# Kernel tuning notes

Hardware: AMD Instinct MI355X
Metric: run time of the kernel (lower is better)

## Reference

```python
import jax, jax.numpy as jnp
import numpy as np
import math

HEAD = 8
D_MODEL = 512
D_K = D_MODEL // HEAD
BS = 1024
HIST = 199


def setup_inputs() -> dict:
    key = jax.random.key(0)
    ks = jax.random.split(key, 9)
    s = 1.0 / math.sqrt(D_MODEL)
    return {
        "current_embed": jax.random.normal(ks[0], (BS, D_MODEL), dtype=jnp.float32),
        "previous_embed": jax.random.normal(ks[1], (BS, HIST, D_MODEL), dtype=jnp.float32),
        "local_attn_mask": jax.random.normal(ks[2], (BS, HIST + 1), dtype=jnp.float32),
        "Wq": jax.random.normal(ks[3], (D_MODEL, D_MODEL), dtype=jnp.float32) * s,
        "bq": jax.random.normal(ks[4], (D_MODEL,), dtype=jnp.float32) * s,
        "Wk": jax.random.normal(ks[5], (D_MODEL, D_MODEL), dtype=jnp.float32) * s,
        "bk": jax.random.normal(ks[6], (D_MODEL,), dtype=jnp.float32) * s,
        "Wv": jax.random.normal(ks[7], (D_MODEL, D_MODEL), dtype=jnp.float32) * s,
        "bv": jax.random.normal(ks[8], (D_MODEL,), dtype=jnp.float32) * s,
    }


def reference(current_embed, previous_embed, local_attn_mask, Wq, bq, Wk, bk, Wv, bv):
    bs = current_embed.shape[0]
    # all_time_embed: [bs, T, d] where T = hist + 1
    all_time = jnp.concatenate([previous_embed, current_embed[:, None, :]], axis=1)
    T = all_time.shape[1]
    # Q: single query per batch -> [bs, head, d_k]
    q = (current_embed @ Wq.T + bq).reshape(bs, HEAD, D_K)
    # K, V over full history -> [bs, T, head, d_k]
    k = (all_time @ Wk.T + bk).reshape(bs, T, HEAD, D_K)
    v = (all_time @ Wv.T + bv).reshape(bs, T, HEAD, D_K)
    # scores: [bs, head, T], scaled; additive mask broadcast over heads
    scores = jnp.einsum("bhd,bthd->bht", q, k) / math.sqrt(D_K)
    norm = jax.nn.softmax(scores + local_attn_mask[:, None, :], axis=-1)
    # weighted sum over time -> [bs, head, d_k] -> [bs, d_model]
    out = jnp.einsum("bht,bthd->bhd", norm, v)
    return out.reshape(bs, D_MODEL)
```

## Files before the change

kernel.cpp:

```cpp
#include <hip/hip_runtime.h>
#include <math.h>

#define DM 512
#define NH 8
#define BS 1024
#define HIST 199
#define TT 200

__device__ __forceinline__ float dot8(const float4& a0, const float4& a1,
                                      const float4& b0, const float4& b1) {
  float p = a0.x * b0.x;
  p = fmaf(a0.y, b0.y, p);
  p = fmaf(a0.z, b0.z, p);
  p = fmaf(a0.w, b0.w, p);
  p = fmaf(a1.x, b1.x, p);
  p = fmaf(a1.y, b1.y, p);
  p = fmaf(a1.z, b1.z, p);
  p = fmaf(a1.w, b1.w, p);
  return p;
}

__device__ __forceinline__ float wred64(float p) {
  p += __shfl_xor(p, 1);
  p += __shfl_xor(p, 2);
  p += __shfl_xor(p, 4);
  p += __shfl_xor(p, 8);
  p += __shfl_xor(p, 16);
  p += __shfl_xor(p, 32);
  return p;
}

__global__ __launch_bounds__(256, 4) void qproj_kernel(
    const float* __restrict__ cur, const float* __restrict__ Wq,
    const float* __restrict__ bq, float* __restrict__ q) {
  const int lane = threadIdx.x & 63;
  const int wave = threadIdx.x >> 6;
  const int bg = blockIdx.x >> 2;
  const int jq = blockIdx.x & 3;
  const int j0 = jq * 128 + wave * 32;
  float4 ca[4], cb[4];
#pragma unroll
  for (int bb = 0; bb < 4; ++bb) {
    const float* cp = cur + (size_t)(bg * 4 + bb) * DM;
    ca[bb] = *(const float4*)(cp + 4 * lane);
    cb[bb] = *(const float4*)(cp + 256 + 4 * lane);
  }
  float keep[2] = {0.f, 0.f};
  for (int r = 0; r < 32; ++r) {
    const float* wp = Wq + (size_t)(j0 + r) * DM;
    const float4 wa = *(const float4*)(wp + 4 * lane);
    const float4 wb = *(const float4*)(wp + 256 + 4 * lane);
    float pp[4];
#pragma unroll
    for (int bb = 0; bb < 4; ++bb)
      pp[bb] = wred64(dot8(ca[bb], cb[bb], wa, wb));
#pragma unroll
    for (int bb = 0; bb < 4; ++bb)
      if (lane == ((bb & 1) * 32 + r)) keep[bb >> 1] = pp[bb];
  }
  const int r = lane & 31, bh = lane >> 5;
  const int j = j0 + r;
#pragma unroll
  for (int s = 0; s < 2; ++s) {
    const int b = bg * 4 + 2 * s + bh;
    q[(size_t)b * DM + j] = keep[s] + bq[j];
  }
}

__global__ __launch_bounds__(256, 4) void qk_kernel(
    const float* __restrict__ q, const float* __restrict__ Wk,
    const float* __restrict__ bk, float* __restrict__ qk1,
    float* __restrict__ qc1) {
  __shared__ float q8[8][64];
  const int tid = threadIdx.x;
  const int bg = blockIdx.x >> 3;
  const int h = blockIdx.x & 7;
  for (int i = tid; i < 512; i += 256) {
    const int bl = i >> 6, d = i & 63;
    q8[bl][d] = q[(size_t)(bg * 8 + bl) * DM + h * 64 + d];
  }
  __syncthreads();
  float acc0[8], acc1[8];
#pragma unroll
  for (int bl = 0; bl < 8; ++bl) {
    acc0[bl] = 0.f;
    acc1[bl] = 0.f;
  }
  const int e = tid;
  const float* wkb = Wk + (size_t)h * 64 * DM;
  for (int d4 = 0; d4 < 64; d4 += 4) {
    float w0[4], w1[4];
#pragma unroll
    for (int dd = 0; dd < 4; ++dd) {
      w0[dd] = wkb[(size_t)(d4 + dd) * DM + e];
      w1[dd] = wkb[(size_t)(d4 + dd) * DM + e + 256];
    }
#pragma unroll
    for (int bl = 0; bl < 8; ++bl) {
      const float4 qq = *(const float4*)&q8[bl][d4];
      acc0[bl] = fmaf(qq.x, w0[0], acc0[bl]);
      acc0[bl] = fmaf(qq.y, w0[1], acc0[bl]);
      acc0[bl] = fmaf(qq.z, w0[2], acc0[bl]);
      acc0[bl] = fmaf(qq.w, w0[3], acc0[bl]);
      acc1[bl] = fmaf(qq.x, w1[0], acc1[bl]);
      acc1[bl] = fmaf(qq.y, w1[1], acc1[bl]);
      acc1[bl] = fmaf(qq.z, w1[2], acc1[bl]);
      acc1[bl] = fmaf(qq.w, w1[3], acc1[bl]);
    }
  }
#pragma unroll
  for (int bl = 0; bl < 8; ++bl) {
    const size_t base = ((size_t)(bg * 8 + bl) * NH + h) * DM;
    qk1[base + e] = acc0[bl] * 0.125f;
    qk1[base + e + 256] = acc1[bl] * 0.125f;
  }
  if (tid < 8) {
    float s = 0.f;
    for (int d = 0; d < 64; ++d) s += q8[tid][d] * bk[h * 64 + d];
    qc1[(size_t)(bg * 8 + tid) * NH + h] = s * 0.125f;
  }
}

__global__ __launch_bounds__(512, 4) void attn_kernel(
    const float* __restrict__ cur, const float* __restrict__ prev,
    const float* __restrict__ mask, const float* __restrict__ qk1,
    const float* __restrict__ qc1, const float* __restrict__ Wv,
    const float* __restrict__ bv, float* __restrict__ out) {
  __shared__ float red[2][4][DM];
  __shared__ float lred[2][4][4];
  const int tid = threadIdx.x;
  const int lane = tid & 63;
  const int wave = tid >> 6;
  const int g = wave & 1;
  const int c = wave >> 1;
  const int b = blockIdx.x;

  float4 ka[4], kb[4];
  float qc[4];
#pragma unroll
  for (int hl = 0; hl < 4; ++hl) {
    const float* kp = qk1 + ((size_t)b * NH + (g * 4 + hl)) * DM;
    ka[hl] = *(const float4*)(kp + 4 * lane);
    kb[hl] = *(const float4*)(kp + 256 + 4 * lane);
    qc[hl] = qc1[(size_t)b * NH + (g * 4 + hl)];
  }
  float4 cA[4], cB[4];
#pragma unroll
  for (int hl = 0; hl < 4; ++hl) {
    cA[hl] = make_float4(0.f, 0.f, 0.f, 0.f);
    cB[hl] = make_float4(0.f, 0.f, 0.f, 0.f);
  }
  float ls0 = 0.f, ls1 = 0.f, ls2 = 0.f, ls3 = 0.f;
  const int t0 = c * 50;
  const int nrows = (c == 3) ? 49 : 50;
  const int ml = (lane < 49) ? lane : 49;
  const float mreg = mask[(size_t)b * TT + t0 + ml];

#define ATTN_ROW(RA, RB, MIDX)                                         \
  {                                                                    \
    float pp[4];                                                       \
    _Pragma("unroll") for (int hl = 0; hl < 4; ++hl) pp[hl] =          \
        dot8(RA, RB, ka[hl], kb[hl]);                                  \
    _Pragma("unroll") for (int hl = 0; hl < 4; ++hl) pp[hl] =          \
        wred64(pp[hl]);                                                \
    const float mval = __shfl(mreg, (MIDX));                           \
    _Pragma("unroll") for (int hl = 0; hl < 4; ++hl) {                 \
      const float w = __expf(pp[hl] + qc[hl] + mval);                  \
      if (hl == 0) ls0 += w;                                           \
      if (hl == 1) ls1 += w;                                           \
      if (hl == 2) ls2 += w;                                           \
      if (hl == 3) ls3 += w;                                           \
      cA[hl].x = fmaf(w, RA.x, cA[hl].x);                              \
      cA[hl].y = fmaf(w, RA.y, cA[hl].y);                              \
      cA[hl].z = fmaf(w, RA.z, cA[hl].z);                              \
      cA[hl].w = fmaf(w, RA.w, cA[hl].w);                              \
      cB[hl].x = fmaf(w, RB.x, cB[hl].x);                              \
      cB[hl].y = fmaf(w, RB.y, cB[hl].y);                              \
      cB[hl].z = fmaf(w, RB.z, cB[hl].z);                              \
      cB[hl].w = fmaf(w, RB.w, cB[hl].w);                              \
    }                                                                  \
  }

  const float* pa = prev + ((size_t)b * HIST + t0) * DM + 4 * lane;
  float4 r0a = *(const float4*)(pa);
  float4 r0b = *(const float4*)(pa + 256);
  float4 r1a = *(const float4*)(pa + DM);
  float4 r1b = *(const float4*)(pa + DM + 256);
  for (int i = 0; i < nrows; ++i) {
    int ip = i + 2;
    if (ip >= nrows) ip = nrows - 1;
    const float* np = pa + (size_t)ip * DM;
    const float4 q0a = *(const float4*)(np);
    const float4 q0b = *(const float4*)(np + 256);
    ATTN_ROW(r0a, r0b, i)
    r0a = r1a;
    r0b = r1b;
    r1a = q0a;
    r1b = q0b;
  }
  if (c == 3) {
    const float* cp = cur + (size_t)b * DM + 4 * lane;
    const float4 xa = *(const float4*)(cp);
    const float4 xb = *(const float4*)(cp + 256);
    ATTN_ROW(xa, xb, 49)
  }
#undef ATTN_ROW

  if (lane == 0) {
    lred[g][c][0] = ls0;
    lred[g][c][1] = ls1;
    lred[g][c][2] = ls2;
    lred[g][c][3] = ls3;
  }
  for (int cc = 0; cc < 4; ++cc) {
    if (c == cc) {
#pragma unroll
      for (int hl = 0; hl < 4; ++hl) {
        float* dst = &red[g][hl][0];
        if (cc == 0) {
          *(float4*)(dst + 4 * lane) = cA[hl];
          *(float4*)(dst + 256 + 4 * lane) = cB[hl];
        } else {
          float4 o0 = *(const float4*)(dst + 4 * lane);
          float4 o1 = *(const float4*)(dst + 256 + 4 * lane);
          o0.x += cA[hl].x;
          o0.y += cA[hl].y;
          o0.z += cA[hl].z;
          o0.w += cA[hl].w;
          o1.x += cB[hl].x;
          o1.y += cB[hl].y;
          o1.z += cB[hl].z;
          o1.w += cB[hl].w;
          *(float4*)(dst + 4 * lane) = o0;
          *(float4*)(dst + 256 + 4 * lane) = o1;
        }
      }
    }
    __syncthreads();
  }
  const int hh = wave;
  const int g2 = hh >> 2, h2 = hh & 3;
  const float linv = 1.0f / (lred[g2][0][h2] + lred[g2][1][h2] +
                             lred[g2][2][h2] + lred[g2][3][h2]);
  const float4 na = *(const float4*)(&red[g2][h2][0] + 4 * lane);
  const float4 nb = *(const float4*)(&red[g2][h2][0] + 256 + 4 * lane);
  float keep = 0.f;
  for (int r = 0; r < 64; ++r) {
    const float* wvp = Wv + (size_t)(hh * 64 + r) * DM;
    const float4 wa = *(const float4*)(wvp + 4 * lane);
    const float4 wb = *(const float4*)(wvp + 256 + 4 * lane);
    float p = wred64(dot8(na, nb, wa, wb));
    if (lane == r) keep = p;
  }
  out[(size_t)b * DM + hh * 64 + lane] = keep * linv + bv[hh * 64 + lane];
}

extern "C" void kernel_launch(void* const* d_in, const int* in_sizes, int n_in,
                              void* d_out, int out_size, void* d_ws,
                              size_t ws_size, hipStream_t stream) {
  const float* cur = (const float*)d_in[0];
  const float* prev = (const float*)d_in[1];
  const float* mask = (const float*)d_in[2];
  const float* Wq = (const float*)d_in[3];
  const float* bq = (const float*)d_in[4];
  const float* Wk = (const float*)d_in[5];
  const float* bk = (const float*)d_in[6];
  const float* Wv = (const float*)d_in[7];
  const float* bv = (const float*)d_in[8];
  float* out = (float*)d_out;

  float* q = (float*)d_ws;
  float* qk1 = q + (size_t)BS * DM;
  float* qc1 = qk1 + (size_t)BS * NH * DM;

  qproj_kernel<<<1024, 256, 0, stream>>>(cur, Wq, bq, q);
  qk_kernel<<<1024, 256, 0, stream>>>(q, Wk, bk, qk1, qc1);
  attn_kernel<<<1024, 512, 0, stream>>>(cur, prev, mask, qk1, qc1, Wv, bv, out);
}
```

Baseline: 681.8 us.

## Batch eight rows per step with transposed butterfly reduction of 32 partial dots

Processes history rows in blocks of 8. The 32 per-(head,row) partial dot products go through a transpose-style butterfly shuffle, so each lane ends up owning one reduced score and computes a single exp. Weights are then broadcast back by shuffle for the V accumulation. This replaces the per-row 4 full 6-step reductions and 4 exps with far fewer shuffles and one exp per lane per block. The cost is reloading each row from global/L2 twice, dropping the software prefetch, and higher register pressure from the 32-element arrays.

```diff
diff --git a/kernel.cpp b/kernel.cpp
--- a/kernel.cpp
+++ b/kernel.cpp
@@ -150,11 +150,78 @@
     cA[hl] = make_float4(0.f, 0.f, 0.f, 0.f);
     cB[hl] = make_float4(0.f, 0.f, 0.f, 0.f);
   }
-  float ls0 = 0.f, ls1 = 0.f, ls2 = 0.f, ls3 = 0.f;
+  float ls[4] = {0.f, 0.f, 0.f, 0.f};
   const int t0 = c * 50;
   const int nrows = (c == 3) ? 49 : 50;
   const int ml = (lane < 49) ? lane : 49;
   const float mreg = mask[(size_t)b * TT + t0 + ml];
+  const float* pa = prev + ((size_t)b * HIST + t0) * DM + 4 * lane;
+
+  const int h_l = (lane >> 3) & 3;
+  const int r_l = lane & 7;
+  const float qc_mine = qc1[(size_t)b * NH + g * 4 + h_l];
+
+  for (int ib = 0; ib < 6; ++ib) {
+    const int i0 = ib * 8;
+    float p[32];
+#pragma unroll
+    for (int rr = 0; rr < 8; ++rr) {
+      const float* rp = pa + (size_t)(i0 + rr) * DM;
+      const float4 ra = *(const float4*)rp;
+      const float4 rb = *(const float4*)(rp + 256);
+#pragma unroll
+      for (int hl = 0; hl < 4; ++hl)
+        p[hl * 8 + rr] = dot8(ra, rb, ka[hl], kb[hl]);
+    }
+    const int s1 = lane & 1, s2 = lane & 2, s4 = lane & 4;
+    const int s8 = lane & 8, s16 = lane & 16;
+    float t16[16];
+#pragma unroll
+    for (int k = 0; k < 16; ++k) {
+      const float a = p[2 * k], bb = p[2 * k + 1];
+      t16[k] = (s1 ? bb : a) + __shfl_xor(s1 ? a : bb, 1);
+    }
+    float t8[8];
+#pragma unroll
+    for (int k = 0; k < 8; ++k) {
+      const float a = t16[2 * k], bb = t16[2 * k + 1];
+      t8[k] = (s2 ? bb : a) + __shfl_xor(s2 ? a : bb, 2);
+    }
+    float t4[4];
+#pragma unroll
+    for (int k = 0; k < 4; ++k) {
+      const float a = t8[2 * k], bb = t8[2 * k + 1];
+      t4[k] = (s4 ? bb : a) + __shfl_xor(s4 ? a : bb, 4);
+    }
+    float t2[2];
+#pragma unroll
+    for (int k = 0; k < 2; ++k) {
+      const float a = t4[2 * k], bb = t4[2 * k + 1];
+      t2[k] = (s8 ? bb : a) + __shfl_xor(s8 ? a : bb, 8);
+    }
+    float sred = (s16 ? t2[1] : t2[0]) + __shfl_xor(s16 ? t2[0] : t2[1], 16);
+    sred += __shfl_xor(sred, 32);
+    const float w_mine = __expf(sred + qc_mine + __shfl(mreg, i0 + r_l));
+#pragma unroll
+    for (int rr = 0; rr < 8; ++rr) {
+      const float* rp = pa + (size_t)(i0 + rr) * DM;
+      const float4 ra = *(const float4*)rp;
+      const float4 rb = *(const float4*)(rp + 256);
+#pragma unroll
+      for (int hl = 0; hl < 4; ++hl) {
+        const float w = __shfl(w_mine, hl * 8 + rr);
+        ls[hl] += w;
+        cA[hl].x = fmaf(w, ra.x, cA[hl].x);
+        cA[hl].y = fmaf(w, ra.y, cA[hl].y);
+        cA[hl].z = fmaf(w, ra.z, cA[hl].z);
+        cA[hl].w = fmaf(w, ra.w, cA[hl].w);
+        cB[hl].x = fmaf(w, rb.x, cB[hl].x);
+        cB[hl].y = fmaf(w, rb.y, cB[hl].y);
+        cB[hl].z = fmaf(w, rb.z, cB[hl].z);
+        cB[hl].w = fmaf(w, rb.w, cB[hl].w);
+      }
+    }
+  }
 
 #define ATTN_ROW(RA, RB, MIDX)                                         \
   {                                                                    \
@@ -166,10 +233,7 @@
     const float mval = __shfl(mreg, (MIDX));                           \
     _Pragma("unroll") for (int hl = 0; hl < 4; ++hl) {                 \
       const float w = __expf(pp[hl] + qc[hl] + mval);                  \
-      if (hl == 0) ls0 += w;                                           \
-      if (hl == 1) ls1 += w;                                           \
-      if (hl == 2) ls2 += w;                                           \
-      if (hl == 3) ls3 += w;                                           \
+      ls[hl] += w;                                                     \
       cA[hl].x = fmaf(w, RA.x, cA[hl].x);                              \
       cA[hl].y = fmaf(w, RA.y, cA[hl].y);                              \
       cA[hl].z = fmaf(w, RA.z, cA[hl].z);                              \
@@ -181,22 +245,11 @@
     }                                                                  \
   }
 
-  const float* pa = prev + ((size_t)b * HIST + t0) * DM + 4 * lane;
-  float4 r0a = *(const float4*)(pa);
-  float4 r0b = *(const float4*)(pa + 256);
-  float4 r1a = *(const float4*)(pa + DM);
-  float4 r1b = *(const float4*)(pa + DM + 256);
-  for (int i = 0; i < nrows; ++i) {
-    int ip = i + 2;
-    if (ip >= nrows) ip = nrows - 1;
-    const float* np = pa + (size_t)ip * DM;
-    const float4 q0a = *(const float4*)(np);
-    const float4 q0b = *(const float4*)(np + 256);
-    ATTN_ROW(r0a, r0b, i)
-    r0a = r1a;
-    r0b = r1b;
-    r1a = q0a;
-    r1b = q0b;
+  for (int i = 48; i < nrows; ++i) {
+    const float* rp = pa + (size_t)i * DM;
+    const float4 ra = *(const float4*)rp;
+    const float4 rb = *(const float4*)(rp + 256);
+    ATTN_ROW(ra, rb, i)
   }
   if (c == 3) {
     const float* cp = cur + (size_t)b * DM + 4 * lane;
@@ -207,10 +260,10 @@
 #undef ATTN_ROW
 
   if (lane == 0) {
-    lred[g][c][0] = ls0;
-    lred[g][c][1] = ls1;
-    lred[g][c][2] = ls2;
-    lred[g][c][3] = ls3;
+    lred[g][c][0] = ls[0];
+    lred[g][c][1] = ls[1];
+    lred[g][c][2] = ls[2];
+    lred[g][c][3] = ls[3];
   }
   for (int cc = 0; cc < 4; ++cc) {
     if (c == cc) {
```

New measurement: 1.069 ms. +56.7%, slower.

## Assign one wave per head over all time steps, dropping cross-wave LDS reduction

Applied to the files above, without the earlier changes.

The attention kernel now gives each of the 8 waves one head and has it walk all 200 time rows, instead of splitting heads into two groups and time into four chunks per wave. This removes the serialized shared-memory reduction of partial context vectors and softmax sums, and the __syncthreads chain that went with it. In exchange, each block now reads every row of previous_embed eight times (once per wave), relying on L1/L2 reuse. The time loop is unrolled by two, the mask is staged in LDS, and launch bounds are raised to 8 blocks per CU for occupancy.

```diff
diff --git a/kernel.cpp b/kernel.cpp
--- a/kernel.cpp
+++ b/kernel.cpp
@@ -121,138 +121,84 @@
   }
 }
 
-__global__ __launch_bounds__(512, 4) void attn_kernel(
+__global__ __launch_bounds__(512, 8) void attn_kernel(
     const float* __restrict__ cur, const float* __restrict__ prev,
     const float* __restrict__ mask, const float* __restrict__ qk1,
     const float* __restrict__ qc1, const float* __restrict__ Wv,
     const float* __restrict__ bv, float* __restrict__ out) {
-  __shared__ float red[2][4][DM];
-  __shared__ float lred[2][4][4];
+  __shared__ float msk[TT];
   const int tid = threadIdx.x;
   const int lane = tid & 63;
-  const int wave = tid >> 6;
-  const int g = wave & 1;
-  const int c = wave >> 1;
+  const int h = tid >> 6;
   const int b = blockIdx.x;
 
-  float4 ka[4], kb[4];
-  float qc[4];
-#pragma unroll
-  for (int hl = 0; hl < 4; ++hl) {
-    const float* kp = qk1 + ((size_t)b * NH + (g * 4 + hl)) * DM;
-    ka[hl] = *(const float4*)(kp + 4 * lane);
-    kb[hl] = *(const float4*)(kp + 256 + 4 * lane);
-    qc[hl] = qc1[(size_t)b * NH + (g * 4 + hl)];
-  }
-  float4 cA[4], cB[4];
-#pragma unroll
-  for (int hl = 0; hl < 4; ++hl) {
-    cA[hl] = make_float4(0.f, 0.f, 0.f, 0.f);
-    cB[hl] = make_float4(0.f, 0.f, 0.f, 0.f);
-  }
-  float ls0 = 0.f, ls1 = 0.f, ls2 = 0.f, ls3 = 0.f;
-  const int t0 = c * 50;
-  const int nrows = (c == 3) ? 49 : 50;
-  const int ml = (lane < 49) ? lane : 49;
-  const float mreg = mask[(size_t)b * TT + t0 + ml];
-
-#define ATTN_ROW(RA, RB, MIDX)                                         \
-  {                                                                    \
-    float pp[4];                                                       \
-    _Pragma("unroll") for (int hl = 0; hl < 4; ++hl) pp[hl] =          \
-        dot8(RA, RB, ka[hl], kb[hl]);                                  \
-    _Pragma("unroll") for (int hl = 0; hl < 4; ++hl) pp[hl] =          \
-        wred64(pp[hl]);                                                \
-    const float mval = __shfl(mreg, (MIDX));                           \
-    _Pragma("unroll") for (int hl = 0; hl < 4; ++hl) {                 \
-      const float w = __expf(pp[hl] + qc[hl] + mval);                  \
-      if (hl == 0) ls0 += w;                                           \
-      if (hl == 1) ls1 += w;                                           \
-      if (hl == 2) ls2 += w;                                           \
-      if (hl == 3) ls3 += w;                                           \
-      cA[hl].x = fmaf(w, RA.x, cA[hl].x);                              \
-      cA[hl].y = fmaf(w, RA.y, cA[hl].y);                              \
-      cA[hl].z = fmaf(w, RA.z, cA[hl].z);                              \
-      cA[hl].w = fmaf(w, RA.w, cA[hl].w);                              \
-      cB[hl].x = fmaf(w, RB.x, cB[hl].x);                              \
-      cB[hl].y = fmaf(w, RB.y, cB[hl].y);                              \
-      cB[hl].z = fmaf(w, RB.z, cB[hl].z);                              \
-      cB[hl].w = fmaf(w, RB.w, cB[hl].w);                              \
-    }                                                                  \
-  }
-
-  const float* pa = prev + ((size_t)b * HIST + t0) * DM + 4 * lane;
+  for (int i = tid; i < TT; i += 512) msk[i] = mask[(size_t)b * TT + i];
+
+  const float* kp = qk1 + ((size_t)b * NH + h) * DM;
+  const float4 ka = *(const float4*)(kp + 4 * lane);
+  const float4 kb = *(const float4*)(kp + 256 + 4 * lane);
+  const float qc = qc1[(size_t)b * NH + h];
+  __syncthreads();
+
+  float4 cA = make_float4(0.f, 0.f, 0.f, 0.f);
+  float4 cB = make_float4(0.f, 0.f, 0.f, 0.f);
+  float ls = 0.f;
+
+#define ATTN_ROW(RA, RB, MV)                        \
+  {                                                 \
+    const float v = wred64(dot8(RA, RB, ka, kb));   \
+    const float w = __expf(v + qc + (MV));          \
+    ls += w;                                        \
+    cA.x = fmaf(w, RA.x, cA.x);                     \
+    cA.y = fmaf(w, RA.y, cA.y);                     \
+    cA.z = fmaf(w, RA.z, cA.z);                     \
+    cA.w = fmaf(w, RA.w, cA.w);                     \
+    cB.x = fmaf(w, RB.x, cB.x);                     \
+    cB.y = fmaf(w, RB.y, cB.y);                     \
+    cB.z = fmaf(w, RB.z, cB.z);                     \
+    cB.w = fmaf(w, RB.w, cB.w);                     \
+  }
+
+  const float* pa = prev + (size_t)b * HIST * DM + 4 * lane;
   float4 r0a = *(const float4*)(pa);
   float4 r0b = *(const float4*)(pa + 256);
   float4 r1a = *(const float4*)(pa + DM);
   float4 r1b = *(const float4*)(pa + DM + 256);
-  for (int i = 0; i < nrows; ++i) {
-    int ip = i + 2;
-    if (ip >= nrows) ip = nrows - 1;
-    const float* np = pa + (size_t)ip * DM;
-    const float4 q0a = *(const float4*)(np);
-    const float4 q0b = *(const float4*)(np + 256);
-    ATTN_ROW(r0a, r0b, i)
-    r0a = r1a;
-    r0b = r1b;
-    r1a = q0a;
-    r1b = q0b;
-  }
-  if (c == 3) {
+  for (int i = 0; i < 198; i += 2) {
+    const float* np0 = pa + (size_t)(i + 2) * DM;
+    int i3 = i + 3;
+    if (i3 > 198) i3 = 198;
+    const float* np1 = pa + (size_t)i3 * DM;
+    const float4 q0a = *(const float4*)(np0);
+    const float4 q0b = *(const float4*)(np0 + 256);
+    const float4 q1a = *(const float4*)(np1);
+    const float4 q1b = *(const float4*)(np1 + 256);
+    ATTN_ROW(r0a, r0b, msk[i])
+    ATTN_ROW(r1a, r1b, msk[i + 1])
+    r0a = q0a;
+    r0b = q0b;
+    r1a = q1a;
+    r1b = q1b;
+  }
+  ATTN_ROW(r0a, r0b, msk[198])
+  {
     const float* cp = cur + (size_t)b * DM + 4 * lane;
     const float4 xa = *(const float4*)(cp);
     const float4 xb = *(const float4*)(cp + 256);
-    ATTN_ROW(xa, xb, 49)
+    ATTN_ROW(xa, xb, msk[199])
   }
 #undef ATTN_ROW
 
-  if (lane == 0) {
-    lred[g][c][0] = ls0;
-    lred[g][c][1] = ls1;
-    lred[g][c][2] = ls2;
-    lred[g][c][3] = ls3;
-  }
-  for (int cc = 0; cc < 4; ++cc) {
-    if (c == cc) {
-#pragma unroll
-      for (int hl = 0; hl < 4; ++hl) {
-        float* dst = &red[g][hl][0];
-        if (cc == 0) {
-          *(float4*)(dst + 4 * lane) = cA[hl];
-          *(float4*)(dst + 256 + 4 * lane) = cB[hl];
-        } else {
-          float4 o0 = *(const float4*)(dst + 4 * lane);
-          float4 o1 = *(const float4*)(dst + 256 + 4 * lane);
-          o0.x += cA[hl].x;
-          o0.y += cA[hl].y;
-          o0.z += cA[hl].z;
-          o0.w += cA[hl].w;
-          o1.x += cB[hl].x;
-          o1.y += cB[hl].y;
-          o1.z += cB[hl].z;
-          o1.w += cB[hl].w;
-          *(float4*)(dst + 4 * lane) = o0;
-          *(float4*)(dst + 256 + 4 * lane) = o1;
-        }
-      }
-    }
-    __syncthreads();
-  }
-  const int hh = wave;
-  const int g2 = hh >> 2, h2 = hh & 3;
-  const float linv = 1.0f / (lred[g2][0][h2] + lred[g2][1][h2] +
-                             lred[g2][2][h2] + lred[g2][3][h2]);
-  const float4 na = *(const float4*)(&red[g2][h2][0] + 4 * lane);
-  const float4 nb = *(const float4*)(&red[g2][h2][0] + 256 + 4 * lane);
+  const float linv = 1.0f / ls;
   float keep = 0.f;
   for (int r = 0; r < 64; ++r) {
-    const float* wvp = Wv + (size_t)(hh * 64 + r) * DM;
+    const float* wvp = Wv + (size_t)(h * 64 + r) * DM;
     const float4 wa = *(const float4*)(wvp + 4 * lane);
     const float4 wb = *(const float4*)(wvp + 256 + 4 * lane);
-    float p = wred64(dot8(na, nb, wa, wb));
+    float p = wred64(dot8(cA, cB, wa, wb));
     if (lane == r) keep = p;
   }
-  out[(size_t)b * DM + hh * 64 + lane] = keep * linv + bv[hh * 64 + lane];
+  out[(size_t)b * DM + h * 64 + lane] = keep * linv + bv[h * 64 + lane];
 }
 
 extern "C" void kernel_launch(void* const* d_in, const int* in_sizes, int n_in,
```

New measurement: 738.2 us. +8.3%, slower.
